# Performance work log

Hardware: AMD Instinct MI355X
Metric: run time of the kernel (lower is better)

The kernel has to match this reference:

```python
import jax, jax.numpy as jnp
import numpy as np

HIDDEN = 1024
TYPE_SIZE = 1000
BATCH = 32
SEQLEN = 512


def setup_inputs() -> dict:
    key = jax.random.key(0)
    k1, k2, k3, k4, k5 = jax.random.split(key, 5)
    event_seqs = jax.random.randint(k1, (BATCH, SEQLEN), 0, TYPE_SIZE + 1)
    duration_seqs = jax.random.uniform(k2, (BATCH, SEQLEN), dtype=jnp.float32)
    # nn.Linear(2H, 7H): weight [7H, 2H], bias [7H]
    bound = 1.0 / np.sqrt(2 * HIDDEN)
    W_rec = jax.random.uniform(k3, (7 * HIDDEN, 2 * HIDDEN), minval=-bound, maxval=bound, dtype=jnp.float32)
    b_rec = jax.random.uniform(k4, (7 * HIDDEN,), minval=-bound, maxval=bound, dtype=jnp.float32)
    emb_table = jax.random.normal(k5, (TYPE_SIZE + 1, HIDDEN), dtype=jnp.float32)
    return {"event_seqs": event_seqs, "duration_seqs": duration_seqs,
            "emb_table": emb_table, "W_rec": W_rec, "b_rec": b_rec}


def _ctlstm_forward(event_seqs, duration_seqs, emb_table, W_rec, b_rec):
    # batch_first=True: transpose to [T, B]
    ev = event_seqs.T          # [T, B]
    dur = duration_seqs.T      # [T, B]
    H = emb_table.shape[1]
    x = emb_table[ev]          # [T, B, H]
    # NOTE: the original forward re-inits h_d/c_d/c_bar to zeros every timestep,
    # so feed = concat(emb_t, zeros) and c_tm1 = c_bar_tm1 = 0: fully parallel in T.
    # rec(feed) with zero h-half == x @ W_rec[:, :H].T + b_rec
    gates = jnp.einsum('tbh,gh->tbg', x, W_rec[:, :H]) + b_rec  # [T, B, 7H]
    gi, gf, gz, go, gib, gfb, gd = jnp.split(gates, 7, axis=-1)
    gi = jax.nn.sigmoid(gi)
    gz = jnp.tanh(gz)
    go = jax.nn.sigmoid(go)
    gib = jax.nn.sigmoid(gib)
    gd = jax.nn.softplus(gd)
    # c_tm1 = 0, c_bar_tm1 = 0
    c = gi * gz                # [T, B, H]
    c_bar = gib * gz           # [T, B, H]
    c_d = c_bar + (c - c_bar) * jnp.exp(-gd * dur[..., None])
    h_d = go * jnp.tanh(c_d)
    return jnp.stack((h_d, c, c_bar, go, gd))  # [5, T, B, H]


def reference(event_seqs, duration_seqs, emb_table, W_rec, b_rec):
    return _ctlstm_forward(event_seqs, duration_seqs, emb_table, W_rec, b_rec)
```

## Files before the change

### kernel.cpp

```cpp
#include <hip/hip_runtime.h>
#include <stdint.h>

#define HID    1024
#define TYPES  1001
#define MPAD   1024
#define NGATES 5120
#define BATCH  32
#define SEQLEN 512
#define TB     (BATCH * SEQLEN)
#define TBH    ((size_t)TB * HID)
#define GSTRIDE ((size_t)MPAD * HID)

typedef __attribute__((ext_vector_type(4))) float  f32x4;
typedef __attribute__((ext_vector_type(8))) __bf16 bf16x8;

__device__ __forceinline__ uint32_t f2bf(float f) {
    uint32_t u = __float_as_uint(f);
    return (u + 0x7FFFu + ((u >> 16) & 1u)) >> 16;
}

__device__ __forceinline__ int gate_off(int g) {
    return (g + (g >= 1) + (g >= 4)) << 10;
}

#define GLD16(gp, lp) __builtin_amdgcn_global_load_lds(                        \
    (const __attribute__((address_space(1))) void*)(uintptr_t)(gp),            \
    (__attribute__((address_space(3))) void*)(uint32_t)(uintptr_t)(lp),        \
    16, 0, 0)

__global__ __launch_bounds__(256) void convert_kernel(
    const float* __restrict__ emb, const float* __restrict__ Wrec,
    uint16_t* __restrict__ Ebf, uint16_t* __restrict__ Wbf)
{
    const int row = blockIdx.x;
    const int tid = threadIdx.x;
    const float* src;
    uint16_t* dst;
    if (row < TYPES) {
        src = emb + (size_t)row * HID;
        dst = Ebf + (size_t)row * HID;
    } else {
        const int n = row - TYPES;
        const int g = n >> 10;
        const int h = n & 1023;
        src = Wrec + (size_t)(gate_off(g) + h) * (2 * HID);
        dst = Wbf + (size_t)n * HID;
    }
    float4 v = ((const float4*)src)[tid];
    uint2 p;
    p.x = f2bf(v.x) | (f2bf(v.y) << 16);
    p.y = f2bf(v.z) | (f2bf(v.w) << 16);
    ((uint2*)dst)[tid] = p;
}

__global__ __launch_bounds__(256) void gemm_gates(
    const uint16_t* __restrict__ E, const uint16_t* __restrict__ W,
    const float* __restrict__ brec, float* __restrict__ G)
{
    __shared__ uint16_t As[128 * 32];
    __shared__ uint16_t Bs[128 * 32];
    const int tM = blockIdx.x;
    const int tN = blockIdx.y;
    const int t = threadIdx.x;
    const int wave = t >> 6;
    const int lane = t & 63;
    const int lane15 = lane & 15;
    const int quad = lane >> 4;
    const int m0 = (wave >> 1) * 64;
    const int n0 = (wave & 1) * 64;

    f32x4 acc[4][4] = {};

    const uint16_t* Ag = E + (size_t)(tM * 128 + (t >> 2)) * HID + (t & 3) * 8;
    const uint16_t* Bg = W + (size_t)(tN * 128 + (t >> 2)) * HID + (t & 3) * 8;
    uint16_t* Al = &As[(t >> 2) * 32 + (t & 3) * 8];
    uint16_t* Bl = &Bs[(t >> 2) * 32 + (t & 3) * 8];

    for (int k0 = 0; k0 < HID; k0 += 32) {
        GLD16(Ag + k0, Al);
        GLD16(Ag + k0 + (size_t)64 * HID, Al + 64 * 32);
        GLD16(Bg + k0, Bl);
        GLD16(Bg + k0 + (size_t)64 * HID, Bl + 64 * 32);
        __syncthreads();

        bf16x8 af[4], bfr[4];
        #pragma unroll
        for (int i = 0; i < 4; i++)
            af[i] = *(const bf16x8*)&As[(m0 + i * 16 + lane15) * 32 + quad * 8];
        #pragma unroll
        for (int i = 0; i < 4; i++)
            bfr[i] = *(const bf16x8*)&Bs[(n0 + i * 16 + lane15) * 32 + quad * 8];

        #pragma unroll
        for (int im = 0; im < 4; im++)
            #pragma unroll
            for (int in = 0; in < 4; in++)
                acc[im][in] = __builtin_amdgcn_mfma_f32_16x16x32_bf16(
                    af[im], bfr[in], acc[im][in], 0, 0, 0);
        __syncthreads();
    }

    #pragma unroll
    for (int in = 0; in < 4; in++) {
        const int n = tN * 128 + n0 + in * 16 + lane15;
        const int g = n >> 10;
        const int h = n & 1023;
        const float bias = brec[gate_off(g) + h];
        float* Gg = G + (size_t)g * GSTRIDE + h;
        #pragma unroll
        for (int im = 0; im < 4; im++) {
            const int mb = tM * 128 + m0 + im * 16 + quad * 4;
            #pragma unroll
            for (int r = 0; r < 4; r++) {
                const float v = acc[im][in][r] + bias;
                float o;
                if (g == 1) {
                    float e = __expf(2.f * v);
                    o = 1.f - 2.f / (e + 1.f);
                } else if (g == 4) {
                    o = fmaxf(v, 0.f) + log1pf(__expf(-fabsf(v)));
                } else {
                    o = 1.f / (1.f + __expf(-v));
                }
                Gg[(size_t)(mb + r) * HID] = o;
            }
        }
    }
}

__global__ __launch_bounds__(256) void expand_kernel(
    const int* __restrict__ ev, const float* __restrict__ dur,
    const float* __restrict__ G, float* __restrict__ out)
{
    const int tb = blockIdx.x;
    const int t = tb >> 5;
    const int b = tb & 31;
    const int src = b * SEQLEN + t;
    const int u = ev[src];
    const float d = dur[src];
    const int tid = threadIdx.x;

    const float* Gu = G + (size_t)u * HID;
    f32x4 gi  = *((const f32x4*)(Gu + 0 * GSTRIDE) + tid);
    f32x4 gz  = *((const f32x4*)(Gu + 1 * GSTRIDE) + tid);
    f32x4 go  = *((const f32x4*)(Gu + 2 * GSTRIDE) + tid);
    f32x4 gib = *((const f32x4*)(Gu + 3 * GSTRIDE) + tid);
    f32x4 gd  = *((const f32x4*)(Gu + 4 * GSTRIDE) + tid);

    f32x4 c, cb, hd;
    #pragma unroll
    for (int j = 0; j < 4; j++) {
        float ci  = gi[j] * gz[j];
        float cbi = gib[j] * gz[j];
        float e   = __expf(-gd[j] * d);
        float cdi = cbi + (ci - cbi) * e;
        float t2  = __expf(2.f * cdi);
        c[j]  = ci;
        cb[j] = cbi;
        hd[j] = go[j] * (1.f - 2.f / (t2 + 1.f));
    }

    float* o = out + (size_t)tb * HID;
    __builtin_nontemporal_store(hd, (f32x4*)(o + 0 * TBH) + tid);
    __builtin_nontemporal_store(c,  (f32x4*)(o + 1 * TBH) + tid);
    __builtin_nontemporal_store(cb, (f32x4*)(o + 2 * TBH) + tid);
    __builtin_nontemporal_store(go, (f32x4*)(o + 3 * TBH) + tid);
    __builtin_nontemporal_store(gd, (f32x4*)(o + 4 * TBH) + tid);
}

extern "C" void kernel_launch(void* const* d_in, const int* in_sizes, int n_in,
                              void* d_out, int out_size, void* d_ws, size_t ws_size,
                              hipStream_t stream) {
    const int*   ev   = (const int*)d_in[0];
    const float* dur  = (const float*)d_in[1];
    const float* emb  = (const float*)d_in[2];
    const float* Wrec = (const float*)d_in[3];
    const float* brec = (const float*)d_in[4];
    float* out = (float*)d_out;

    char* ws = (char*)d_ws;
    uint16_t* Ebf = (uint16_t*)ws;
    uint16_t* Wbf = (uint16_t*)(ws + (size_t)2 * 1024 * 1024);
    float*    G   = (float*)(ws + (size_t)12 * 1024 * 1024);

    convert_kernel<<<dim3(TYPES + NGATES), dim3(256), 0, stream>>>(emb, Wrec, Ebf, Wbf);
    gemm_gates<<<dim3(8, 40), dim3(256), 0, stream>>>(Ebf, Wbf, brec, G);
    expand_kernel<<<dim3(TB), dim3(256), 0, stream>>>(ev, dur, G, out);
}
```

Baseline: 466.0 us.

## Fuse gate products into GEMM epilogue with double-buffered swizzled tiles

Each GEMM block now computes all five gates for the same hidden columns, so its epilogue can precompute c = gi*gz and c_bar = gib*gz. It writes four planes instead of five, which cuts table writes and the gathered reads in the expand kernel. The GEMM main loop moves to BK=64 with double-buffered LDS, an XOR-swizzled layout to avoid bank conflicts, and a 128x160 tile. The grid shrinks from 320 to 256 blocks, which may lower occupancy. The expand kernel is dominated by its output writes, so the total gain is limited.

```diff
diff --git a/kernel.cpp b/kernel.cpp
--- a/kernel.cpp
+++ b/kernel.cpp
@@ -4,12 +4,16 @@
 #define HID    1024
 #define TYPES  1001
 #define MPAD   1024
+#define PLANE  ((size_t)MPAD * HID)
 #define NGATES 5120
 #define BATCH  32
 #define SEQLEN 512
 #define TB     (BATCH * SEQLEN)
 #define TBH    ((size_t)TB * HID)
-#define GSTRIDE ((size_t)MPAD * HID)
+
+#define BK 64
+#define TM 128
+#define TNH 32
 
 typedef __attribute__((ext_vector_type(4))) float  f32x4;
 typedef __attribute__((ext_vector_type(8))) __bf16 bf16x8;
@@ -55,82 +59,104 @@
 
 __global__ __launch_bounds__(256) void gemm_gates(
     const uint16_t* __restrict__ E, const uint16_t* __restrict__ W,
-    const float* __restrict__ brec, float* __restrict__ G)
+    const float* __restrict__ brec, float* __restrict__ G4)
 {
-    __shared__ uint16_t As[128 * 32];
-    __shared__ uint16_t Bs[128 * 32];
-    const int tM = blockIdx.x;
-    const int tN = blockIdx.y;
+    __shared__ uint16_t As[2][TM * BK];
+    __shared__ uint16_t Bs[2][160 * BK];
+    const int tMb = blockIdx.x;
+    const int tNb = blockIdx.y;
     const int t = threadIdx.x;
     const int wave = t >> 6;
     const int lane = t & 63;
     const int lane15 = lane & 15;
     const int quad = lane >> 4;
     const int m0 = (wave >> 1) * 64;
-    const int n0 = (wave & 1) * 64;
-
-    f32x4 acc[4][4] = {};
-
-    const uint16_t* Ag = E + (size_t)(tM * 128 + (t >> 2)) * HID + (t & 3) * 8;
-    const uint16_t* Bg = W + (size_t)(tN * 128 + (t >> 2)) * HID + (t & 3) * 8;
-    uint16_t* Al = &As[(t >> 2) * 32 + (t & 3) * 8];
-    uint16_t* Bl = &Bs[(t >> 2) * 32 + (t & 3) * 8];
-
-    for (int k0 = 0; k0 < HID; k0 += 32) {
-        GLD16(Ag + k0, Al);
-        GLD16(Ag + k0 + (size_t)64 * HID, Al + 64 * 32);
-        GLD16(Bg + k0, Bl);
-        GLD16(Bg + k0 + (size_t)64 * HID, Bl + 64 * 32);
+    const int n0h = (wave & 1) * 16;
+
+    const int rA = t >> 3;
+    const int csrc = (t & 7) ^ (rA & 7);
+    const uint16_t* Ag = E + (size_t)(tMb * TM + rA) * HID + csrc * 8;
+    const uint16_t* Bg = W + (size_t)(tNb * TNH + rA) * HID + csrc * 8;
+
+    const int l7 = lane15 & 7;
+    const int pc0 = ((0 | quad) ^ l7) * 8;
+    const int pc1 = ((4 | quad) ^ l7) * 8;
+
+    f32x4 acc[4][5] = {};
+
+#define STAGE(buf, k0) do {                                                      \
+        _Pragma("unroll")                                                        \
+        for (int r = 0; r < 4; ++r)                                              \
+            GLD16(Ag + (k0) + (size_t)(r * 32) * HID, &As[buf][r * 2048 + t * 8]); \
+        _Pragma("unroll")                                                        \
+        for (int r = 0; r < 5; ++r)                                              \
+            GLD16(Bg + (k0) + (size_t)(r * 1024) * HID, &Bs[buf][r * 2048 + t * 8]); \
+    } while (0)
+
+    STAGE(0, 0);
+    __syncthreads();
+
+    int cur = 0;
+    for (int kt = 0; kt < 16; ++kt) {
+        if (kt < 15) STAGE(cur ^ 1, (kt + 1) * BK);
+        const uint16_t* Ac = As[cur];
+        const uint16_t* Bc = Bs[cur];
+        #pragma unroll
+        for (int kk = 0; kk < 2; ++kk) {
+            const int pc = kk ? pc1 : pc0;
+            bf16x8 af[4], bv[5];
+            #pragma unroll
+            for (int im = 0; im < 4; ++im)
+                af[im] = *(const bf16x8*)&Ac[(m0 + im * 16 + lane15) * BK + pc];
+            #pragma unroll
+            for (int in = 0; in < 5; ++in)
+                bv[in] = *(const bf16x8*)&Bc[(in * 32 + n0h + lane15) * BK + pc];
+            #pragma unroll
+            for (int im = 0; im < 4; ++im)
+                #pragma unroll
+                for (int in = 0; in < 5; ++in)
+                    acc[im][in] = __builtin_amdgcn_mfma_f32_16x16x32_bf16(
+                        af[im], bv[in], acc[im][in], 0, 0, 0);
+        }
         __syncthreads();
-
-        bf16x8 af[4], bfr[4];
+        cur ^= 1;
+    }
+#undef STAGE
+
+    const int h = tNb * TNH + n0h + lane15;
+    const float b0 = brec[0    + h];
+    const float b1 = brec[2048 + h];
+    const float b2 = brec[3072 + h];
+    const float b3 = brec[4096 + h];
+    const float b4 = brec[6144 + h];
+    #pragma unroll
+    for (int im = 0; im < 4; ++im) {
+        const int mb = tMb * TM + m0 + im * 16 + quad * 4;
         #pragma unroll
-        for (int i = 0; i < 4; i++)
-            af[i] = *(const bf16x8*)&As[(m0 + i * 16 + lane15) * 32 + quad * 8];
-        #pragma unroll
-        for (int i = 0; i < 4; i++)
-            bfr[i] = *(const bf16x8*)&Bs[(n0 + i * 16 + lane15) * 32 + quad * 8];
-
-        #pragma unroll
-        for (int im = 0; im < 4; im++)
-            #pragma unroll
-            for (int in = 0; in < 4; in++)
-                acc[im][in] = __builtin_amdgcn_mfma_f32_16x16x32_bf16(
-                    af[im], bfr[in], acc[im][in], 0, 0, 0);
-        __syncthreads();
-    }
-
-    #pragma unroll
-    for (int in = 0; in < 4; in++) {
-        const int n = tN * 128 + n0 + in * 16 + lane15;
-        const int g = n >> 10;
-        const int h = n & 1023;
-        const float bias = brec[gate_off(g) + h];
-        float* Gg = G + (size_t)g * GSTRIDE + h;
-        #pragma unroll
-        for (int im = 0; im < 4; im++) {
-            const int mb = tM * 128 + m0 + im * 16 + quad * 4;
-            #pragma unroll
-            for (int r = 0; r < 4; r++) {
-                const float v = acc[im][in][r] + bias;
-                float o;
-                if (g == 1) {
-                    float e = __expf(2.f * v);
-                    o = 1.f - 2.f / (e + 1.f);
-                } else if (g == 4) {
-                    o = fmaxf(v, 0.f) + log1pf(__expf(-fabsf(v)));
-                } else {
-                    o = 1.f / (1.f + __expf(-v));
-                }
-                Gg[(size_t)(mb + r) * HID] = o;
-            }
+        for (int r = 0; r < 4; ++r) {
+            const float vi  = acc[im][0][r] + b0;
+            const float vz  = acc[im][1][r] + b1;
+            const float vo  = acc[im][2][r] + b2;
+            const float vib = acc[im][3][r] + b3;
+            const float vd  = acc[im][4][r] + b4;
+            const float gi  = 1.f / (1.f + __expf(-vi));
+            const float ez  = __expf(2.f * vz);
+            const float gz  = 1.f - 2.f / (ez + 1.f);
+            const float go  = 1.f / (1.f + __expf(-vo));
+            const float gib = 1.f / (1.f + __expf(-vib));
+            const float gd  = fmaxf(vd, 0.f) + log1pf(__expf(-fabsf(vd)));
+            const size_t base = (size_t)(mb + r) * HID + h;
+            G4[0 * PLANE + base] = gi * gz;
+            G4[1 * PLANE + base] = gib * gz;
+            G4[2 * PLANE + base] = go;
+            G4[3 * PLANE + base] = gd;
         }
     }
 }
 
 __global__ __launch_bounds__(256) void expand_kernel(
     const int* __restrict__ ev, const float* __restrict__ dur,
-    const float* __restrict__ G, float* __restrict__ out)
+    const float* __restrict__ G4, float* __restrict__ out)
 {
     const int tb = blockIdx.x;
     const int t = tb >> 5;
@@ -140,23 +166,18 @@
     const float d = dur[src];
     const int tid = threadIdx.x;
 
-    const float* Gu = G + (size_t)u * HID;
-    f32x4 gi  = *((const f32x4*)(Gu + 0 * GSTRIDE) + tid);
-    f32x4 gz  = *((const f32x4*)(Gu + 1 * GSTRIDE) + tid);
-    f32x4 go  = *((const f32x4*)(Gu + 2 * GSTRIDE) + tid);
-    f32x4 gib = *((const f32x4*)(Gu + 3 * GSTRIDE) + tid);
-    f32x4 gd  = *((const f32x4*)(Gu + 4 * GSTRIDE) + tid);
-
-    f32x4 c, cb, hd;
+    const float* Gu = G4 + (size_t)u * HID;
+    f32x4 c  = *((const f32x4*)(Gu + 0 * PLANE) + tid);
+    f32x4 cb = *((const f32x4*)(Gu + 1 * PLANE) + tid);
+    f32x4 go = *((const f32x4*)(Gu + 2 * PLANE) + tid);
+    f32x4 gd = *((const f32x4*)(Gu + 3 * PLANE) + tid);
+
+    f32x4 hd;
     #pragma unroll
     for (int j = 0; j < 4; j++) {
-        float ci  = gi[j] * gz[j];
-        float cbi = gib[j] * gz[j];
         float e   = __expf(-gd[j] * d);
-        float cdi = cbi + (ci - cbi) * e;
+        float cdi = cb[j] + (c[j] - cb[j]) * e;
         float t2  = __expf(2.f * cdi);
-        c[j]  = ci;
-        cb[j] = cbi;
         hd[j] = go[j] * (1.f - 2.f / (t2 + 1.f));
     }
 
@@ -181,9 +202,9 @@
     char* ws = (char*)d_ws;
     uint16_t* Ebf = (uint16_t*)ws;
     uint16_t* Wbf = (uint16_t*)(ws + (size_t)2 * 1024 * 1024);
-    float*    G   = (float*)(ws + (size_t)12 * 1024 * 1024);
+    float*    G4  = (float*)(ws + (size_t)12 * 1024 * 1024);
 
     convert_kernel<<<dim3(TYPES + NGATES), dim3(256), 0, stream>>>(emb, Wrec, Ebf, Wbf);
-    gemm_gates<<<dim3(8, 40), dim3(256), 0, stream>>>(Ebf, Wbf, brec, G);
-    expand_kernel<<<dim3(TB), dim3(256), 0, stream>>>(ev, dur, G, out);
-}
+    gemm_gates<<<dim3(8, 32), dim3(256), 0, stream>>>(Ebf, Wbf, brec, G4);
+    expand_kernel<<<dim3(TB), dim3(256), 0, stream>>>(ev, dur, G4, out);
+}
```

New measurement: 417.3 us. 10.5% less time.
